# Kernel tuning notes

Measured on AMD Instinct MI355X. Metric: run time of the kernel, lower is better.

## Reference

```python
import jax, jax.numpy as jnp
import numpy as np

N_NODES = 50000
N_FEAT = 128
N_EDGES = 600000
HIDDEN = 256  # hidden_dim
IN_DIM = 2 * N_FEAT
LEAKY_SLOPE = 0.01  # torch LeakyReLU default


def setup_inputs() -> dict:
    key = jax.random.key(0)
    ks = jax.random.split(key, 8)
    x = jax.random.normal(ks[0], (N_NODES, N_FEAT), dtype=jnp.float32)
    edge_index = jax.random.randint(ks[1], (2, N_EDGES), 0, N_NODES, dtype=jnp.int64 if jax.config.jax_enable_x64 else jnp.int32)
    # Linear params, torch default init scale ~ 1/sqrt(fan_in)
    def lin(k, fan_in, fan_out):
        k1, k2 = jax.random.split(k)
        bound = 1.0 / np.sqrt(fan_in)
        W = jax.random.uniform(k1, (fan_in, fan_out), minval=-bound, maxval=bound, dtype=jnp.float32)
        b = jax.random.uniform(k2, (fan_out,), minval=-bound, maxval=bound, dtype=jnp.float32)
        return W, b
    W1, b1 = lin(ks[2], IN_DIM, HIDDEN)
    W2, b2 = lin(ks[3], HIDDEN, HIDDEN // 2)
    W3, b3 = lin(ks[4], HIDDEN // 2, 1)
    return {"x": x, "edge_index": edge_index,
            "W1": W1, "b1": b1, "W2": W2, "b2": b2, "W3": W3, "b3": b3}


def reference(x, edge_index, W1, b1, W2, b2, W3, b3):
    row, col = edge_index[0], edge_index[1]
    # gather + concat: [E, 2F]
    combined = jnp.concatenate([x[row], x[col]], axis=1)
    h = jax.nn.relu(combined @ W1 + b1)               # [E, H] (dropout: eval mode, identity)
    h = jax.nn.leaky_relu(h @ W2 + b2, negative_slope=LEAKY_SLOPE)  # [E, H//2]
    out = (h @ W3 + b3).squeeze(-1)                   # [E]
    return out
```

## Files before the change

kernel.cpp:

```cpp
#include <hip/hip_runtime.h>
#include <hip/hip_bf16.h>

#define NNODES 50000
#define NFEAT  128
#define NEDGES 600000
#define HID    256
#define HID2   128
#define LEAKY  0.01f

typedef __attribute__((ext_vector_type(8))) short short8;
typedef __attribute__((ext_vector_type(4))) float floatx4;

__device__ __forceinline__ void split_bf16(float x, unsigned short& hi, unsigned short& lo) {
  union { float f; unsigned u; } a; a.f = x;
  hi = (unsigned short)(a.u >> 16);
  union { float f; unsigned u; } h; h.u = (unsigned)hi << 16;
  union { float f; unsigned u; } r; r.f = x - h.f;
  lo = (unsigned short)(r.u >> 16);
}

__device__ __forceinline__ unsigned short bf16_rne(float x) {
  union { float f; unsigned u; } a; a.f = x;
  unsigned r = a.u + 0x7FFFu + ((a.u >> 16) & 1u);
  return (unsigned short)(r >> 16);
}

__device__ __forceinline__ unsigned pack2_rne(float a, float b) {
  __hip_bfloat162 h = __float22bfloat162_rn(make_float2(a, b));
  unsigned u; __builtin_memcpy(&u, &h, 4); return u;
}

__device__ __forceinline__ float ubits2f(unsigned u) {
  union { unsigned u; float f; } c; c.u = u; return c.f;
}

__device__ __forceinline__ unsigned fuse2(unsigned pw, unsigned qw) {
  const float a0 = ubits2f(pw << 16), a1 = ubits2f(pw & 0xFFFF0000u);
  const float c0 = ubits2f(qw << 16), c1 = ubits2f(qw & 0xFFFF0000u);
  return pack2_rne(fmaxf(a0 + c0, 0.f), fmaxf(a1 + c1, 0.f));
}

__global__ __launch_bounds__(256) void pack_w(const float* __restrict__ W2,
                                              const float* __restrict__ W1,
                                              unsigned short* __restrict__ W2F,
                                              unsigned short* __restrict__ W1F) {
  const int gid = blockIdx.x * 256 + threadIdx.x;
  if (gid < 32768) {
    const int idx = gid;
    const int i  = idx & 7;
    const int l  = (idx >> 3) & 63;
    const int nf = (idx >> 9) & 7;
    const int ks = idx >> 12;
    const int k   = ks * 32 + (l >> 4) * 8 + i;
    const int col = nf * 16 + (l & 15);
    W2F[idx] = bf16_rne(W2[k * HID2 + col]);
  } else if (gid < 32768 + 65536) {
    const int idx = gid - 32768;
    const int i  = idx & 7;
    const int l  = (idx >> 3) & 63;
    const int nf = (idx >> 9) & 31;
    const int ks = idx >> 14;
    const int k = ks * 32 + (l >> 4) * 8 + i;
    const int n = nf * 16 + (l & 15);
    const float v = (n < 256) ? W1[k * HID + n] : W1[(128 + k) * HID + (n - 256)];
    unsigned short hi, lo;
    split_bf16(v, hi, lo);
    W1F[idx]         = hi;
    W1F[65536 + idx] = lo;
  }
}

__global__ __launch_bounds__(256) void pq_mfma(
    const float* __restrict__ x, const unsigned short* __restrict__ W1F,
    const float* __restrict__ b1,
    unsigned short* __restrict__ Pb, unsigned short* __restrict__ Qb) {
  const int bid   = blockIdx.x;
  const int nhalf = bid & 1;
  const int n0    = (bid >> 1) * 64;
  const int t     = threadIdx.x;

  __shared__ __align__(16) unsigned short sbuf[2][64 * 128];
  unsigned short* xhi = sbuf[0];
  unsigned short* xlo = sbuf[1];

#pragma unroll
  for (int rep = 0; rep < 8; ++rep) {
    const int flat = rep * 1024 + t * 4;
    const int row = flat >> 7, f0 = flat & 127;
    float4 v = make_float4(0.f, 0.f, 0.f, 0.f);
    if (n0 + row < NNODES)
      v = *reinterpret_cast<const float4*>(&x[(size_t)(n0 + row) * NFEAT + f0]);
    unsigned short h[4], l[4];
    split_bf16(v.x, h[0], l[0]); split_bf16(v.y, h[1], l[1]);
    split_bf16(v.z, h[2], l[2]); split_bf16(v.w, h[3], l[3]);
    const unsigned bt = (unsigned)(row * 256) +
                        (((unsigned)(2 * f0)) ^ (((unsigned)(row & 7)) << 4));
    *reinterpret_cast<uint2*>(reinterpret_cast<char*>(xhi) + bt) =
        make_uint2((unsigned)h[0] | ((unsigned)h[1] << 16),
                   (unsigned)h[2] | ((unsigned)h[3] << 16));
    *reinterpret_cast<uint2*>(reinterpret_cast<char*>(xlo) + bt) =
        make_uint2((unsigned)l[0] | ((unsigned)l[1] << 16),
                   (unsigned)l[2] | ((unsigned)l[3] << 16));
  }
  __syncthreads();

  const int wid = t >> 6, lane = t & 63;
  const int rg = wid >> 1, cg = wid & 1;
  const int lr = lane & 15, kc = lane >> 4;

  floatx4 acc[2][8];
#pragma unroll
  for (int mf = 0; mf < 2; ++mf)
#pragma unroll
    for (int nf = 0; nf < 8; ++nf) acc[mf][nf] = (floatx4)0.f;

#pragma unroll
  for (int ks = 0; ks < 4; ++ks) {
    short8 ah[2], al[2];
#pragma unroll
    for (int mf = 0; mf < 2; ++mf) {
      const int row = rg * 32 + mf * 16 + lr;
      const unsigned bt = (unsigned)(row * 256) +
                          (((unsigned)(ks * 64 + kc * 16)) ^ (((unsigned)(row & 7)) << 4));
      ah[mf] = *reinterpret_cast<const short8*>(reinterpret_cast<const char*>(xhi) + bt);
      al[mf] = *reinterpret_cast<const short8*>(reinterpret_cast<const char*>(xlo) + bt);
    }
#pragma unroll
    for (int nf = 0; nf < 8; ++nf) {
      const int nfg = nhalf * 16 + cg * 8 + nf;
      const size_t off = ((size_t)(ks * 32 + nfg) * 64 + lane) * 8;
      const short8 bh = *reinterpret_cast<const short8*>(W1F + off);
      const short8 bl = *reinterpret_cast<const short8*>(W1F + 65536 + off);
#pragma unroll
      for (int mf = 0; mf < 2; ++mf) {
        acc[mf][nf] = __builtin_amdgcn_mfma_f32_16x16x32_bf16(ah[mf], bh, acc[mf][nf], 0, 0, 0);
        acc[mf][nf] = __builtin_amdgcn_mfma_f32_16x16x32_bf16(ah[mf], bl, acc[mf][nf], 0, 0, 0);
        acc[mf][nf] = __builtin_amdgcn_mfma_f32_16x16x32_bf16(al[mf], bh, acc[mf][nf], 0, 0, 0);
      }
    }
  }

  float bias[8];
#pragma unroll
  for (int nf = 0; nf < 8; ++nf)
    bias[nf] = (nhalf == 0) ? b1[cg * 128 + nf * 16 + lr] : 0.f;

  __syncthreads();
  unsigned short* stg = &sbuf[0][0];
#pragma unroll
  for (int mf = 0; mf < 2; ++mf)
#pragma unroll
    for (int nf = 0; nf < 8; ++nf)
#pragma unroll
      for (int r = 0; r < 4; ++r) {
        const int rl = rg * 32 + mf * 16 + kc * 4 + r;
        const int cl = cg * 128 + nf * 16 + lr;
        stg[rl * 256 + cl] = bf16_rne(acc[mf][nf][r] + bias[nf]);
      }
  __syncthreads();

  unsigned short* dst = (nhalf == 0) ? Pb : Qb;
#pragma unroll
  for (int rep = 0; rep < 8; ++rep) {
    const int i = rep * 256 + t;
    const int row = i >> 5, colu = i & 31;
    if (n0 + row < NNODES)
      *reinterpret_cast<uint4*>(reinterpret_cast<char*>(dst) +
                                (size_t)(n0 + row) * 512 + colu * 16) =
          *reinterpret_cast<const uint4*>(reinterpret_cast<const char*>(stg) +
                                          row * 512 + colu * 16);
  }
}

__global__ __launch_bounds__(256) void edge_mlp_mfma9(
    const int* __restrict__ ei,
    const unsigned short* __restrict__ W2F, const float* __restrict__ b2,
    const float* __restrict__ W3, const float* __restrict__ b3,
    const unsigned short* __restrict__ Pb, const unsigned short* __restrict__ Qb,
    float* __restrict__ out) {
  const int t  = threadIdx.x;
  const int e0 = blockIdx.x * 64;
  const int wid = t >> 6, lane = t & 63;

  __shared__ __align__(16) unsigned short h1s[64 * 256];
  __shared__ float outs[4][32];

  const int rv = ei[e0 + wid * 16 + (lane & 15)];
  const int cv = ei[NEDGES + e0 + wid * 16 + (lane & 15)];
  const char* Pc = reinterpret_cast<const char*>(Pb);
  const char* Qc = reinterpret_cast<const char*>(Qb);
  const unsigned vo = (unsigned)(lane * 8);

  uint2 P0[8], Q0[8], P1[8], Q1[8];
#pragma unroll
  for (int j = 0; j < 8; ++j) {
    const int r = __builtin_amdgcn_readlane(rv, j);
    const int c = __builtin_amdgcn_readlane(cv, j);
    P0[j] = *reinterpret_cast<const uint2*>(Pc + (size_t)r * 512 + vo);
    Q0[j] = *reinterpret_cast<const uint2*>(Qc + (size_t)c * 512 + vo);
  }
#pragma unroll
  for (int j = 0; j < 8; ++j) {
    const int r = __builtin_amdgcn_readlane(rv, 8 + j);
    const int c = __builtin_amdgcn_readlane(cv, 8 + j);
    P1[j] = *reinterpret_cast<const uint2*>(Pc + (size_t)r * 512 + vo);
    Q1[j] = *reinterpret_cast<const uint2*>(Qc + (size_t)c * 512 + vo);
  }

#pragma unroll
  for (int j = 0; j < 8; ++j) {
    const int e = wid * 16 + j;
    const unsigned bt = (unsigned)(e * 512) + (vo ^ (((unsigned)(e & 7)) << 4));
    *reinterpret_cast<uint2*>(reinterpret_cast<char*>(h1s) + bt) =
        make_uint2(fuse2(P0[j].x, Q0[j].x), fuse2(P0[j].y, Q0[j].y));
  }
#pragma unroll
  for (int j = 0; j < 8; ++j) {
    const int e = wid * 16 + 8 + j;
    const unsigned bt = (unsigned)(e * 512) + (vo ^ (((unsigned)(e & 7)) << 4));
    *reinterpret_cast<uint2*>(reinterpret_cast<char*>(h1s) + bt) =
        make_uint2(fuse2(P1[j].x, Q1[j].x), fuse2(P1[j].y, Q1[j].y));
  }
  __syncthreads();

  const int wr = wid >> 1, wc = wid & 1;
  const int lr = lane & 15, kc = lane >> 4;

  floatx4 acc[2][4];
#pragma unroll
  for (int mf = 0; mf < 2; ++mf)
#pragma unroll
    for (int nf = 0; nf < 4; ++nf) acc[mf][nf] = (floatx4)0.f;

#pragma unroll
  for (int ks = 0; ks < 8; ++ks) {
    short8 ah[2];
#pragma unroll
    for (int mf = 0; mf < 2; ++mf) {
      const int row = wr * 32 + mf * 16 + lr;
      const unsigned bt = (unsigned)(row * 512) +
                          (((unsigned)(ks * 64 + kc * 16)) ^ (((unsigned)(row & 7)) << 4));
      ah[mf] = *reinterpret_cast<const short8*>(reinterpret_cast<const char*>(h1s) + bt);
    }
    short8 bh[4];
#pragma unroll
    for (int nf = 0; nf < 4; ++nf) {
      const unsigned off = (unsigned)(((ks * 8 + wc * 4 + nf) * 64 + lane) * 8);
      bh[nf] = *reinterpret_cast<const short8*>(W2F + off);
    }
#pragma unroll
    for (int mf = 0; mf < 2; ++mf)
#pragma unroll
      for (int nf = 0; nf < 4; ++nf)
        acc[mf][nf] = __builtin_amdgcn_mfma_f32_16x16x32_bf16(ah[mf], bh[nf], acc[mf][nf], 0, 0, 0);
  }

  float w3v[4], b2v[4];
#pragma unroll
  for (int nf = 0; nf < 4; ++nf) {
    const int col = wc * 64 + nf * 16 + lr;
    w3v[nf] = W3[col];
    b2v[nf] = b2[col];
  }

  float part[2][4];
#pragma unroll
  for (int mf = 0; mf < 2; ++mf)
#pragma unroll
    for (int r = 0; r < 4; ++r) {
      float s = 0.f;
#pragma unroll
      for (int nf = 0; nf < 4; ++nf) {
        float h = acc[mf][nf][r] + b2v[nf];
        h = (h > 0.f) ? h : LEAKY * h;
        s = fmaf(h, w3v[nf], s);
      }
      part[mf][r] = s;
    }

#pragma unroll
  for (int m = 1; m <= 8; m <<= 1)
#pragma unroll
    for (int mf = 0; mf < 2; ++mf)
#pragma unroll
      for (int r = 0; r < 4; ++r) part[mf][r] += __shfl_xor(part[mf][r], m, 64);

  if (lr == 0) {
#pragma unroll
    for (int mf = 0; mf < 2; ++mf)
#pragma unroll
      for (int r = 0; r < 4; ++r) outs[wid][mf * 16 + kc * 4 + r] = part[mf][r];
  }
  __syncthreads();

  if (t < 64) {
    const int wrg = t >> 5;
    out[e0 + t] = outs[wrg * 2][t & 31] + outs[wrg * 2 + 1][t & 31] + b3[0];
  }
}

__global__ __launch_bounds__(256) void edge_mlp_direct(
    const float* __restrict__ x, const int* __restrict__ ei,
    const float* __restrict__ W1, const float* __restrict__ b1,
    const float* __restrict__ W2, const float* __restrict__ b2,
    const float* __restrict__ W3, const float* __restrict__ b3,
    float* __restrict__ out) {
  const int t  = threadIdx.x;
  const int e0 = blockIdx.x * 32;

  __shared__ __align__(16) float h1f[32 * HID];
  __shared__ int eidx[2][32];

  if (t < 32)      eidx[0][t]      = ei[e0 + t];
  else if (t < 64) eidx[1][t - 32] = ei[NEDGES + e0 + (t - 32)];
  __syncthreads();

  const float b1r = b1[t];
  __shared__ float xr[32][128];
  __shared__ float xc[32][128];
  for (int idx = t; idx < 32 * 128; idx += 256) {
    const int e = idx >> 7, f = idx & 127;
    xr[e][f] = x[(size_t)eidx[0][e] * NFEAT + f];
    xc[e][f] = x[(size_t)eidx[1][e] * NFEAT + f];
  }
  __syncthreads();
  float s[32];
#pragma unroll
  for (int e = 0; e < 32; ++e) s[e] = b1r;
  for (int f = 0; f < 128; ++f) {
    const float wr = W1[f * HID + t];
    const float wb = W1[(128 + f) * HID + t];
#pragma unroll
    for (int e = 0; e < 32; ++e)
      s[e] = fmaf(xr[e][f], wr, fmaf(xc[e][f], wb, s[e]));
  }
#pragma unroll
  for (int e = 0; e < 32; ++e) h1f[e * HID + t] = fmaxf(s[e], 0.f);
  __syncthreads();

  const int tr = t >> 5;
  const int tc = t & 31;
  float acc[4][4];
#pragma unroll
  for (int i = 0; i < 4; ++i)
#pragma unroll
    for (int j = 0; j < 4; ++j) acc[i][j] = 0.f;

  const float4* __restrict__ W2v = reinterpret_cast<const float4*>(W2);
  const float4* __restrict__ h1v = reinterpret_cast<const float4*>(h1f);
  for (int k = 0; k < HID; k += 4) {
    float4 a[4];
#pragma unroll
    for (int i = 0; i < 4; ++i) a[i] = h1v[((4 * tr + i) * HID + k) >> 2];
    float4 b[4];
#pragma unroll
    for (int kk = 0; kk < 4; ++kk) b[kk] = W2v[(k + kk) * 32 + tc];
#pragma unroll
    for (int i = 0; i < 4; ++i) {
      const float* av = reinterpret_cast<const float*>(&a[i]);
#pragma unroll
      for (int kk = 0; kk < 4; ++kk) {
        const float* bv = reinterpret_cast<const float*>(&b[kk]);
#pragma unroll
        for (int j = 0; j < 4; ++j) acc[i][j] = fmaf(av[kk], bv[j], acc[i][j]);
      }
    }
  }

  float w3r[4], b2r[4];
#pragma unroll
  for (int j = 0; j < 4; ++j) {
    w3r[j] = W3[4 * tc + j];
    b2r[j] = b2[4 * tc + j];
  }
  const float b3v = b3[0];
  float partial[4];
#pragma unroll
  for (int i = 0; i < 4; ++i) {
    float sp = 0.f;
#pragma unroll
    for (int j = 0; j < 4; ++j) {
      float h = acc[i][j] + b2r[j];
      h = (h > 0.f) ? h : LEAKY * h;
      sp = fmaf(h, w3r[j], sp);
    }
    partial[i] = sp;
  }
#pragma unroll
  for (int m = 16; m >= 1; m >>= 1)
#pragma unroll
    for (int i = 0; i < 4; ++i) partial[i] += __shfl_xor(partial[i], m, 32);
  if (tc == 0) {
#pragma unroll
    for (int i = 0; i < 4; ++i) out[e0 + 4 * tr + i] = partial[i] + b3v;
  }
}

extern "C" void kernel_launch(void* const* d_in, const int* in_sizes, int n_in,
                              void* d_out, int out_size, void* d_ws, size_t ws_size,
                              hipStream_t stream) {
  const float* x  = (const float*)d_in[0];
  const int*   ei = (const int*)d_in[1];
  const float* W1 = (const float*)d_in[2];
  const float* b1 = (const float*)d_in[3];
  const float* W2 = (const float*)d_in[4];
  const float* b2 = (const float*)d_in[5];
  const float* W3 = (const float*)d_in[6];
  const float* b3 = (const float*)d_in[7];
  float* out = (float*)d_out;

  const size_t p_bytes   = (size_t)NNODES * 256 * 2;
  const size_t w2f_bytes = (size_t)32768 * 2;
  const size_t w1f_bytes = (size_t)2 * 65536 * 2;
  const size_t need = 2 * p_bytes + w2f_bytes + w1f_bytes;

  if (ws_size >= need) {
    unsigned short* Pb  = (unsigned short*)d_ws;
    unsigned short* Qb  = (unsigned short*)((char*)d_ws + p_bytes);
    unsigned short* W2F = (unsigned short*)((char*)d_ws + 2 * p_bytes);
    unsigned short* W1F = (unsigned short*)((char*)d_ws + 2 * p_bytes + w2f_bytes);

    pack_w<<<(32768 + 65536 + 255) / 256, 256, 0, stream>>>(W2, W1, W2F, W1F);
    const int pq_blocks = ((NNODES + 63) / 64) * 2;
    pq_mfma<<<pq_blocks, 256, 0, stream>>>(x, W1F, b1, Pb, Qb);
    edge_mlp_mfma9<<<NEDGES / 64, 256, 0, stream>>>(ei, W2F, b2, W3, b3, Pb, Qb, out);
  } else {
    edge_mlp_direct<<<NEDGES / 32, 256, 0, stream>>>(x, ei, W1, b1, W2, b2, W3, b3, out);
  }
}
```

Baseline: 147.1 us.

## Sort edges by source row before edge MLP to localize P gathers

Adds a counting-sort pipeline (histogram, single-block scan, atomic scatter) that reorders edges by row index. The edge MLP kernel then reads the sorted row/col arrays and writes each result through a permutation. The intent is cache locality for the P-row gathers, since consecutive edges share source nodes. It adds three kernels, a memset, atomics and a scattered output store.

```diff
diff --git a/kernel.cpp b/kernel.cpp
--- a/kernel.cpp
+++ b/kernel.cpp
@@ -7,6 +7,7 @@
 #define HID    256
 #define HID2   128
 #define LEAKY  0.01f
+#define NBINS  50176
 
 typedef __attribute__((ext_vector_type(8))) short short8;
 typedef __attribute__((ext_vector_type(4))) float floatx4;
@@ -38,6 +39,56 @@
   const float a0 = ubits2f(pw << 16), a1 = ubits2f(pw & 0xFFFF0000u);
   const float c0 = ubits2f(qw << 16), c1 = ubits2f(qw & 0xFFFF0000u);
   return pack2_rne(fmaxf(a0 + c0, 0.f), fmaxf(a1 + c1, 0.f));
+}
+
+__global__ __launch_bounds__(256) void hist_rows(const int* __restrict__ ei,
+                                                 int* __restrict__ cnt) {
+  const int e = blockIdx.x * 256 + threadIdx.x;
+  if (e < NEDGES) atomicAdd(&cnt[ei[e]], 1);
+}
+
+__global__ __launch_bounds__(1024) void scan_offsets(const int* __restrict__ cnt,
+                                                     int* __restrict__ cur) {
+  __shared__ int ssum[1024];
+  const int t = threadIdx.x;
+  int s = 0;
+#pragma unroll
+  for (int i = 0; i < 49; ++i) {
+    const int b = t * 49 + i;
+    s += (b < NNODES) ? cnt[b] : 0;
+  }
+  ssum[t] = s;
+  __syncthreads();
+  for (int d = 1; d < 1024; d <<= 1) {
+    const int v = (t >= d) ? ssum[t - d] : 0;
+    __syncthreads();
+    ssum[t] += v;
+    __syncthreads();
+  }
+  int base = (t == 0) ? 0 : ssum[t - 1];
+#pragma unroll
+  for (int i = 0; i < 49; ++i) {
+    const int b = t * 49 + i;
+    if (b < NNODES) {
+      cur[b] = base;
+      base += cnt[b];
+    }
+  }
+}
+
+__global__ __launch_bounds__(256) void scatter_edges(const int* __restrict__ ei,
+                                                     int* __restrict__ cur,
+                                                     int* __restrict__ sr,
+                                                     int* __restrict__ sc,
+                                                     int* __restrict__ pm) {
+  const int e = blockIdx.x * 256 + threadIdx.x;
+  if (e < NEDGES) {
+    const int r = ei[e], c = ei[NEDGES + e];
+    const int pos = atomicAdd(&cur[r], 1);
+    sr[pos] = r;
+    sc[pos] = c;
+    pm[pos] = e;
+  }
 }
 
 __global__ __launch_bounds__(256) void pack_w(const float* __restrict__ W2,
@@ -172,8 +223,9 @@
   }
 }
 
-__global__ __launch_bounds__(256) void edge_mlp_mfma9(
-    const int* __restrict__ ei,
+__global__ __launch_bounds__(256) void edge_mlp_mfma10(
+    const int* __restrict__ sr, const int* __restrict__ sc,
+    const int* __restrict__ pm,
     const unsigned short* __restrict__ W2F, const float* __restrict__ b2,
     const float* __restrict__ W3, const float* __restrict__ b3,
     const unsigned short* __restrict__ Pb, const unsigned short* __restrict__ Qb,
@@ -185,8 +237,8 @@
   __shared__ __align__(16) unsigned short h1s[64 * 256];
   __shared__ float outs[4][32];
 
-  const int rv = ei[e0 + wid * 16 + (lane & 15)];
-  const int cv = ei[NEDGES + e0 + wid * 16 + (lane & 15)];
+  const int rv = sr[e0 + wid * 16 + (lane & 15)];
+  const int cv = sc[e0 + wid * 16 + (lane & 15)];
   const char* Pc = reinterpret_cast<const char*>(Pb);
   const char* Qc = reinterpret_cast<const char*>(Qb);
   const unsigned vo = (unsigned)(lane * 8);
@@ -295,7 +347,8 @@
 
   if (t < 64) {
     const int wrg = t >> 5;
-    out[e0 + t] = outs[wrg * 2][t & 31] + outs[wrg * 2 + 1][t & 31] + b3[0];
+    const float v = outs[wrg * 2][t & 31] + outs[wrg * 2 + 1][t & 31] + b3[0];
+    out[pm[e0 + t]] = v;
   }
 }
 
@@ -412,18 +465,34 @@
   const size_t p_bytes   = (size_t)NNODES * 256 * 2;
   const size_t w2f_bytes = (size_t)32768 * 2;
   const size_t w1f_bytes = (size_t)2 * 65536 * 2;
-  const size_t need = 2 * p_bytes + w2f_bytes + w1f_bytes;
+  const size_t e_bytes   = (size_t)NEDGES * 4;
+  const size_t c_bytes   = (size_t)NBINS * 4;
+  const size_t need = 2 * p_bytes + w2f_bytes + w1f_bytes +
+                      3 * e_bytes + 2 * c_bytes;
 
   if (ws_size >= need) {
-    unsigned short* Pb  = (unsigned short*)d_ws;
-    unsigned short* Qb  = (unsigned short*)((char*)d_ws + p_bytes);
-    unsigned short* W2F = (unsigned short*)((char*)d_ws + 2 * p_bytes);
-    unsigned short* W1F = (unsigned short*)((char*)d_ws + 2 * p_bytes + w2f_bytes);
+    char* p = (char*)d_ws;
+    unsigned short* Pb  = (unsigned short*)p;            p += p_bytes;
+    unsigned short* Qb  = (unsigned short*)p;            p += p_bytes;
+    unsigned short* W2F = (unsigned short*)p;            p += w2f_bytes;
+    unsigned short* W1F = (unsigned short*)p;            p += w1f_bytes;
+    int* sr  = (int*)p;                                  p += e_bytes;
+    int* sc  = (int*)p;                                  p += e_bytes;
+    int* pm  = (int*)p;                                  p += e_bytes;
+    int* cnt = (int*)p;                                  p += c_bytes;
+    int* cur = (int*)p;
+
+    hipMemsetAsync(cnt, 0, c_bytes, stream);
+    hist_rows<<<(NEDGES + 255) / 256, 256, 0, stream>>>(ei, cnt);
+    scan_offsets<<<1, 1024, 0, stream>>>(cnt, cur);
+    scatter_edges<<<(NEDGES + 255) / 256, 256, 0, stream>>>(ei, cur, sr, sc, pm);
 
     pack_w<<<(32768 + 65536 + 255) / 256, 256, 0, stream>>>(W2, W1, W2F, W1F);
     const int pq_blocks = ((NNODES + 63) / 64) * 2;
     pq_mfma<<<pq_blocks, 256, 0, stream>>>(x, W1F, b1, Pb, Qb);
-    edge_mlp_mfma9<<<NEDGES / 64, 256, 0, stream>>>(ei, W2F, b2, W3, b3, Pb, Qb, out);
+
+    edge_mlp_mfma10<<<NEDGES / 64, 256, 0, stream>>>(sr, sc, pm, W2F, b2, W3, b3,
+                                                     Pb, Qb, out);
   } else {
     edge_mlp_direct<<<NEDGES / 32, 256, 0, stream>>>(x, ei, W1, b1, W2, b2, W3, b3, out);
   }
```

Measured after the change: 290.2 us. 1.97x slower.
